# Performance work log

Hardware: AMD Instinct MI355X
Metric: run time of the kernel (lower is better)

Reference implementation:

```python
import jax, jax.numpy as jnp
import numpy as np

N = 1024
DIM = 128
HEADS = 8
DK = DIM // HEADS
EDIM = 16
EPS = 1e-5
NEG = -10000.0


def _lin(k, din, dout):
    return jax.random.normal(k, (din, dout), jnp.float32) * (1.0 / np.sqrt(din))


def setup_inputs() -> dict:
    key = jax.random.key(0)
    ks = jax.random.split(key, 10)
    mask = jax.random.randint(ks[2], (N, N), 0, 2).astype(bool)
    mask = mask | jnp.eye(N, dtype=bool)  # self-loops always valid
    return {
        "x": jax.random.normal(ks[0], (N, DIM), jnp.float32),
        "edge_feat": jax.random.normal(ks[1], (N, N, EDIM), jnp.float32),
        "mask": mask,
        "Wq": _lin(ks[3], DIM, DIM), "bq": jnp.zeros((DIM,), jnp.float32),
        "Wk": _lin(ks[4], DIM, DIM), "bk": jnp.zeros((DIM,), jnp.float32),
        "Wv": _lin(ks[5], DIM, DIM), "bv": jnp.zeros((DIM,), jnp.float32),
        "Wae": _lin(ks[6], EDIM, HEADS), "bae": jnp.zeros((HEADS,), jnp.float32),
        "Wve": _lin(ks[7], EDIM, DIM), "bve": jnp.zeros((DIM,), jnp.float32),
        "Wo": _lin(ks[8], DIM, DIM), "bo": jnp.zeros((DIM,), jnp.float32),
        "gamma": jnp.ones((DIM,), jnp.float32),
        "beta": jnp.zeros((DIM,), jnp.float32),
    }


def reference(x, edge_feat, mask, Wq, bq, Wk, bk, Wv, bv, Wae, bae, Wve, bve, Wo, bo, gamma, beta):
    n, dim = x.shape
    heads = bae.shape[0]
    dk = dim // heads
    # pre-LayerNorm
    mu = jnp.mean(x, axis=-1, keepdims=True)
    var = jnp.mean(jnp.square(x - mu), axis=-1, keepdims=True)
    h = (x - mu) * jax.lax.rsqrt(var + EPS) * gamma + beta
    q = (h @ Wq + bq).reshape(n, heads, dk)
    k = (h @ Wk + bk).reshape(n, heads, dk)
    v = (h @ Wv + bv).reshape(n, heads, dk)
    # attention logits with per-edge additive bias: (n, m, heads)
    att = jnp.einsum('nhd,mhd->nmh', q, k) / np.sqrt(dk).astype(np.float32)
    att = att + edge_feat @ Wae + bae
    att = jnp.where(mask[..., None], att, NEG)
    alpha = jax.nn.softmax(att, axis=1)  # softmax over source nodes m
    # edge-conditioned values: msg_{nm} = v_m + U(e_{nm})
    edge_val = (edge_feat @ Wve + bve).reshape(n, n, heads, dk)
    out = jnp.einsum('nmh,mhd->nhd', alpha, v) + jnp.einsum('nmh,nmhd->nhd', alpha, edge_val)
    out = out.reshape(n, dim) @ Wo + bo
    return x + out
```

## Files before the change

### kernel.cpp

```cpp
#include <hip/hip_runtime.h>
#include <hip/hip_bf16.h>

#define NNODE 1024
#define DIM 128
#define HEADS 8
#define DK 16
#define EDIM 16
#define BN 8
#define MR 32
#define KV_ROW 160
#define H_STRIDE 20
#define EF_ROW 20
#define EF_NSTR 644
#define LOG2E 1.44269504f

__global__ __launch_bounds__(384)
void ln_qkv_kernel(const float* __restrict__ x,
                   const float* __restrict__ Wq, const float* __restrict__ bq,
                   const float* __restrict__ Wk, const float* __restrict__ bk,
                   const float* __restrict__ Wv, const float* __restrict__ bv,
                   const float* __restrict__ gamma, const float* __restrict__ beta,
                   float* __restrict__ qg, float* __restrict__ kg, float* __restrict__ vg) {
    const int n = blockIdx.x;
    const int t = threadIdx.x;
    __shared__ float hrow[DIM];
    __shared__ float part[4];

    float xv = 0.f;
    if (t < 128) {
        xv = x[n * DIM + t];
        float v = xv;
        #pragma unroll
        for (int off = 32; off >= 1; off >>= 1) v += __shfl_xor(v, off);
        if ((t & 63) == 0) part[t >> 6] = v;
    }
    __syncthreads();
    const float mu = (part[0] + part[1]) * (1.0f / DIM);
    const float dx = xv - mu;
    if (t < 128) {
        float v = dx * dx;
        #pragma unroll
        for (int off = 32; off >= 1; off >>= 1) v += __shfl_xor(v, off);
        if ((t & 63) == 0) part[2 + (t >> 6)] = v;
    }
    __syncthreads();
    if (t < 128) {
        const float var = (part[2] + part[3]) * (1.0f / DIM);
        hrow[t] = dx * rsqrtf(var + 1e-5f) * gamma[t] + beta[t];
    }
    __syncthreads();

    const int which = t >> 7;
    const int col = t & 127;
    const float* W = (which == 0) ? Wq : (which == 1) ? Wk : Wv;
    const float* b = (which == 0) ? bq : (which == 1) ? bk : bv;
    float* o       = (which == 0) ? qg : (which == 1) ? kg : vg;
    float acc = b[col];
    #pragma unroll 16
    for (int i = 0; i < DIM; ++i) acc = fmaf(hrow[i], W[i * DIM + col], acc);
    o[n * DIM + col] = acc;
}

__global__ __launch_bounds__(256, 2)
void attn_kernel(const float* __restrict__ qg, const float* __restrict__ kg,
                 const float* __restrict__ vg, const float* __restrict__ ef,
                 const int* __restrict__ mask,
                 const float* __restrict__ Wae, const float* __restrict__ bae,
                 float* __restrict__ acc) {
    const int t = threadIdx.x;
    const int s  = t >> 5;
    const int np = (t >> 3) & 3;
    const int h  = t & 7;
    const int wid = t >> 6, lane = t & 63;
    const int bx = blockIdx.x;
    const int n0 = (bx >> 5) * BN;
    const int mb = (bx & 31) * MR;

    __shared__ float ef_lds[BN * EF_NSTR];
    __shared__ float kv_buf[2 * MR * KV_ROW];
    __shared__ int   mk_lds[BN * 34];

    float* k_lds = kv_buf;
    float* v_lds = kv_buf + MR * KV_ROW;

    #pragma unroll
    for (int r = 0; r < 4; ++r) {
        const int idx = t + 256 * r;
        const int nn = idx >> 7;
        const int mm = (idx >> 2) & 31;
        const int q4 = idx & 3;
        const float4 ev = *(const float4*)(ef + ((size_t)(n0 + nn) * NNODE + mb + mm) * EDIM + q4 * 4);
        *(float4*)&ef_lds[nn * EF_NSTR + mm * EF_ROW + q4 * 4] = ev;
    }
    #pragma unroll
    for (int r = 0; r < 4; ++r) {
        const int idx = t + 256 * r;
        const int mm = idx >> 5, c4 = idx & 31;
        const int hh = c4 >> 2, d4 = c4 & 3;
        const float4 kq = *(const float4*)(kg + (size_t)(mb + mm) * DIM + c4 * 4);
        const float4 vq = *(const float4*)(vg + (size_t)(mb + mm) * DIM + c4 * 4);
        *(float4*)&k_lds[mm * KV_ROW + hh * H_STRIDE + d4 * 4] = kq;
        *(float4*)&v_lds[mm * KV_ROW + hh * H_STRIDE + d4 * 4] = vq;
    }
    {
        const int nn = t >> 5, mm = t & 31;
        mk_lds[nn * 34 + mm] = mask[(size_t)(n0 + nn) * NNODE + (mb + mm)];
    }
    float qreg[2][DK];
    #pragma unroll
    for (int hf = 0; hf < 2; ++hf) {
        const float* qp = qg + (size_t)(n0 + np + 4 * hf) * DIM + h * DK;
        #pragma unroll
        for (int d4 = 0; d4 < 4; ++d4) {
            const float4 qv = *(const float4*)(qp + d4 * 4);
            qreg[hf][d4 * 4 + 0] = qv.x; qreg[hf][d4 * 4 + 1] = qv.y;
            qreg[hf][d4 * 4 + 2] = qv.z; qreg[hf][d4 * 4 + 3] = qv.w;
        }
    }
    float waec[EDIM];
    #pragma unroll
    for (int e = 0; e < EDIM; ++e) waec[e] = Wae[e * HEADS + h] * LOG2E;
    const float baeh = bae[h] * LOG2E;

    float sl[2] = {0.f, 0.f};
    float accv[2][DK], accT[2][EDIM];
    #pragma unroll
    for (int hf = 0; hf < 2; ++hf) {
        #pragma unroll
        for (int d = 0; d < DK; ++d) accv[hf][d] = 0.f;
        #pragma unroll
        for (int e = 0; e < EDIM; ++e) accT[hf][e] = 0.f;
    }

    __syncthreads();

    #pragma unroll
    for (int j = 0; j < 4; ++j) {
        const int m = j * 8 + s;
        float kk[DK], vv[DK];
        const float* kp = &k_lds[m * KV_ROW + h * H_STRIDE];
        const float* vp = &v_lds[m * KV_ROW + h * H_STRIDE];
        #pragma unroll
        for (int d4 = 0; d4 < 4; ++d4) {
            const float4 k4 = *(const float4*)(kp + d4 * 4);
            kk[d4 * 4 + 0] = k4.x; kk[d4 * 4 + 1] = k4.y;
            kk[d4 * 4 + 2] = k4.z; kk[d4 * 4 + 3] = k4.w;
            const float4 v4 = *(const float4*)(vp + d4 * 4);
            vv[d4 * 4 + 0] = v4.x; vv[d4 * 4 + 1] = v4.y;
            vv[d4 * 4 + 2] = v4.z; vv[d4 * 4 + 3] = v4.w;
        }
        #pragma unroll
        for (int hf = 0; hf < 2; ++hf) {
            const int n = np + 4 * hf;
            const float* ep = &ef_lds[n * EF_NSTR + m * EF_ROW];
            float efv[EDIM];
            #pragma unroll
            for (int e4 = 0; e4 < 4; ++e4) {
                const float4 ev = *(const float4*)(ep + e4 * 4);
                efv[e4 * 4 + 0] = ev.x; efv[e4 * 4 + 1] = ev.y;
                efv[e4 * 4 + 2] = ev.z; efv[e4 * 4 + 3] = ev.w;
            }
            float bias = baeh, dot = 0.f;
            #pragma unroll
            for (int e = 0; e < EDIM; ++e) bias = fmaf(efv[e], waec[e], bias);
            #pragma unroll
            for (int d = 0; d < DK; ++d) dot = fmaf(qreg[hf][d], kk[d], dot);
            const float lg = fmaf(dot, 0.25f * LOG2E, bias);
            const float p = mk_lds[n * 34 + m] ? __builtin_amdgcn_exp2f(lg) : 0.f;
            sl[hf] += p;
            #pragma unroll
            for (int d = 0; d < DK; ++d) accv[hf][d] = fmaf(p, vv[d], accv[hf][d]);
            #pragma unroll
            for (int e = 0; e < EDIM; ++e) accT[hf][e] = fmaf(p, efv[e], accT[hf][e]);
        }
    }

    #pragma unroll
    for (int hf = 0; hf < 2; ++hf) {
        sl[hf] += __shfl_xor(sl[hf], 32);
        #pragma unroll
        for (int d = 0; d < DK; ++d) accv[hf][d] += __shfl_xor(accv[hf][d], 32);
        #pragma unroll
        for (int e = 0; e < EDIM; ++e) accT[hf][e] += __shfl_xor(accT[hf][e], 32);
    }
    __syncthreads();
    float* red = kv_buf;
    if (lane < 32) {
        float* rp = &red[((wid * 4 + np) * 8 + h) * 66];
        #pragma unroll
        for (int hf = 0; hf < 2; ++hf) {
            rp[hf * 33 + 0] = sl[hf];
            #pragma unroll
            for (int d = 0; d < DK; ++d) rp[hf * 33 + 1 + d] = accv[hf][d];
            #pragma unroll
            for (int e = 0; e < EDIM; ++e) rp[hf * 33 + 17 + e] = accT[hf][e];
        }
    }
    __syncthreads();
    for (int v = t; v < BN * HEADS * 33; v += 256) {
        const int n = v / 264;
        const int rem = v - n * 264;
        const int hh = rem / 33;
        const int idx = rem - hh * 33;
        const int nnp = n & 3, hf = n >> 2;
        float sum = 0.f;
        #pragma unroll
        for (int w = 0; w < 4; ++w)
            sum += red[((w * 4 + nnp) * 8 + hh) * 66 + hf * 33 + idx];
        atomicAdd(&acc[((size_t)(n0 + n) * HEADS + hh) * 33 + idx], sum);
    }
}

__global__ __launch_bounds__(128)
void final_kernel(const float* __restrict__ acc,
                  const float* __restrict__ Wve, const float* __restrict__ bve,
                  const float* __restrict__ x,
                  const float* __restrict__ Wo, const float* __restrict__ bo,
                  float* __restrict__ out) {
    const int n = blockIdx.x, t = threadIdx.x;
    __shared__ float ab[HEADS * 33];
    __shared__ float orow[DIM];
    for (int u = t; u < HEADS * 33; u += 128) ab[u] = acc[(size_t)n * HEADS * 33 + u];
    __syncthreads();
    const int col = t, hh = col >> 4, dd = col & 15;
    const float slv = ab[hh * 33];
    float acc2 = 0.f;
    #pragma unroll
    for (int e = 0; e < EDIM; ++e) acc2 = fmaf(ab[hh * 33 + 17 + e], Wve[e * DIM + col], acc2);
    orow[col] = (ab[hh * 33 + 1 + dd] + acc2) / slv + bve[col];
    __syncthreads();
    float o = bo[col] + x[(size_t)n * DIM + col];
    #pragma unroll 16
    for (int i = 0; i < DIM; ++i) o = fmaf(orow[i], Wo[i * DIM + col], o);
    out[(size_t)n * DIM + col] = o;
}

extern "C" void kernel_launch(void* const* d_in, const int* in_sizes, int n_in,
                              void* d_out, int out_size, void* d_ws, size_t ws_size,
                              hipStream_t stream) {
    const float* x     = (const float*)d_in[0];
    const float* ef    = (const float*)d_in[1];
    const int*   mask  = (const int*)d_in[2];
    const float* Wq    = (const float*)d_in[3];
    const float* bq    = (const float*)d_in[4];
    const float* Wk    = (const float*)d_in[5];
    const float* bk    = (const float*)d_in[6];
    const float* Wv    = (const float*)d_in[7];
    const float* bv    = (const float*)d_in[8];
    const float* Wae   = (const float*)d_in[9];
    const float* bae   = (const float*)d_in[10];
    const float* Wve   = (const float*)d_in[11];
    const float* bve   = (const float*)d_in[12];
    const float* Wo    = (const float*)d_in[13];
    const float* bo    = (const float*)d_in[14];
    const float* gamma = (const float*)d_in[15];
    const float* beta  = (const float*)d_in[16];

    float* ws = (float*)d_ws;
    float* accb = ws;
    float* qg   = ws + 270336;
    float* kg   = qg + (size_t)NNODE * DIM;
    float* vg   = kg + (size_t)NNODE * DIM;

    hipMemsetAsync(accb, 0, (size_t)NNODE * HEADS * 33 * sizeof(float), stream);
    ln_qkv_kernel<<<NNODE, 384, 0, stream>>>(x, Wq, bq, Wk, bk, Wv, bv, gamma, beta, qg, kg, vg);
    attn_kernel<<<(NNODE / BN) * 32, 256, 0, stream>>>(qg, kg, vg, ef, mask, Wae, bae, accb);
    final_kernel<<<NNODE, 128, 0, stream>>>(accb, Wve, bve, x, Wo, bo, (float*)d_out);
}
```

Baseline: 184.8 us.

## Loop attention blocks over 8 source chunks with smaller LDS tiles and higher occupancy

Each attention block now walks 8 chunks of 16 source nodes instead of handling one 32-node tile. The grid drops from 4096 to 1024 blocks, so fewer partial results get atomically accumulated. LDS per block shrinks and launch bounds ask for 4 blocks per CU to raise occupancy, at the cost of a sync per chunk and no overlap between loads and compute. The projection GEMV loops also split their FMA chains into two accumulators to add ILP.

```diff
diff --git a/kernel.cpp b/kernel.cpp
--- a/kernel.cpp
+++ b/kernel.cpp
@@ -7,12 +7,18 @@
 #define DK 16
 #define EDIM 16
 #define BN 8
-#define MR 32
+#define MR 16
+#define NCH 8
 #define KV_ROW 160
 #define H_STRIDE 20
 #define EF_ROW 20
-#define EF_NSTR 644
+#define EF_NSTR 324
+#define MK_STR 17
 #define LOG2E 1.44269504f
+
+#define SMEM_F 8448
+#define KV_OFF 2592
+#define MK_OFF 7712
 
 __global__ __launch_bounds__(384)
 void ln_qkv_kernel(const float* __restrict__ x,
@@ -55,13 +61,16 @@
     const float* W = (which == 0) ? Wq : (which == 1) ? Wk : Wv;
     const float* b = (which == 0) ? bq : (which == 1) ? bk : bv;
     float* o       = (which == 0) ? qg : (which == 1) ? kg : vg;
-    float acc = b[col];
-    #pragma unroll 16
-    for (int i = 0; i < DIM; ++i) acc = fmaf(hrow[i], W[i * DIM + col], acc);
-    o[n * DIM + col] = acc;
-}
-
-__global__ __launch_bounds__(256, 2)
+    float a0 = b[col], a1 = 0.f;
+    #pragma unroll 8
+    for (int i = 0; i < DIM; i += 2) {
+        a0 = fmaf(hrow[i],     W[i * DIM + col],       a0);
+        a1 = fmaf(hrow[i + 1], W[(i + 1) * DIM + col], a1);
+    }
+    o[n * DIM + col] = a0 + a1;
+}
+
+__global__ __launch_bounds__(256, 4)
 void attn_kernel(const float* __restrict__ qg, const float* __restrict__ kg,
                  const float* __restrict__ vg, const float* __restrict__ ef,
                  const int* __restrict__ mask,
@@ -73,39 +82,15 @@
     const int h  = t & 7;
     const int wid = t >> 6, lane = t & 63;
     const int bx = blockIdx.x;
-    const int n0 = (bx >> 5) * BN;
-    const int mb = (bx & 31) * MR;
-
-    __shared__ float ef_lds[BN * EF_NSTR];
-    __shared__ float kv_buf[2 * MR * KV_ROW];
-    __shared__ int   mk_lds[BN * 34];
-
-    float* k_lds = kv_buf;
-    float* v_lds = kv_buf + MR * KV_ROW;
-
-    #pragma unroll
-    for (int r = 0; r < 4; ++r) {
-        const int idx = t + 256 * r;
-        const int nn = idx >> 7;
-        const int mm = (idx >> 2) & 31;
-        const int q4 = idx & 3;
-        const float4 ev = *(const float4*)(ef + ((size_t)(n0 + nn) * NNODE + mb + mm) * EDIM + q4 * 4);
-        *(float4*)&ef_lds[nn * EF_NSTR + mm * EF_ROW + q4 * 4] = ev;
-    }
-    #pragma unroll
-    for (int r = 0; r < 4; ++r) {
-        const int idx = t + 256 * r;
-        const int mm = idx >> 5, c4 = idx & 31;
-        const int hh = c4 >> 2, d4 = c4 & 3;
-        const float4 kq = *(const float4*)(kg + (size_t)(mb + mm) * DIM + c4 * 4);
-        const float4 vq = *(const float4*)(vg + (size_t)(mb + mm) * DIM + c4 * 4);
-        *(float4*)&k_lds[mm * KV_ROW + hh * H_STRIDE + d4 * 4] = kq;
-        *(float4*)&v_lds[mm * KV_ROW + hh * H_STRIDE + d4 * 4] = vq;
-    }
-    {
-        const int nn = t >> 5, mm = t & 31;
-        mk_lds[nn * 34 + mm] = mask[(size_t)(n0 + nn) * NNODE + (mb + mm)];
-    }
+    const int n0  = (bx >> 3) * BN;
+    const int mb0 = (bx & 7) * (MR * NCH);
+
+    __shared__ float smem[SMEM_F];
+    float* ef_lds = smem;
+    float* k_lds  = smem + KV_OFF;
+    float* v_lds  = smem + KV_OFF + MR * KV_ROW;
+    int*   mk_lds = (int*)(smem + MK_OFF);
+
     float qreg[2][DK];
     #pragma unroll
     for (int hf = 0; hf < 2; ++hf) {
@@ -132,46 +117,75 @@
         for (int e = 0; e < EDIM; ++e) accT[hf][e] = 0.f;
     }
 
-    __syncthreads();
-
-    #pragma unroll
-    for (int j = 0; j < 4; ++j) {
-        const int m = j * 8 + s;
-        float kk[DK], vv[DK];
-        const float* kp = &k_lds[m * KV_ROW + h * H_STRIDE];
-        const float* vp = &v_lds[m * KV_ROW + h * H_STRIDE];
-        #pragma unroll
-        for (int d4 = 0; d4 < 4; ++d4) {
-            const float4 k4 = *(const float4*)(kp + d4 * 4);
-            kk[d4 * 4 + 0] = k4.x; kk[d4 * 4 + 1] = k4.y;
-            kk[d4 * 4 + 2] = k4.z; kk[d4 * 4 + 3] = k4.w;
-            const float4 v4 = *(const float4*)(vp + d4 * 4);
-            vv[d4 * 4 + 0] = v4.x; vv[d4 * 4 + 1] = v4.y;
-            vv[d4 * 4 + 2] = v4.z; vv[d4 * 4 + 3] = v4.w;
-        }
-        #pragma unroll
-        for (int hf = 0; hf < 2; ++hf) {
-            const int n = np + 4 * hf;
-            const float* ep = &ef_lds[n * EF_NSTR + m * EF_ROW];
-            float efv[EDIM];
-            #pragma unroll
-            for (int e4 = 0; e4 < 4; ++e4) {
-                const float4 ev = *(const float4*)(ep + e4 * 4);
-                efv[e4 * 4 + 0] = ev.x; efv[e4 * 4 + 1] = ev.y;
-                efv[e4 * 4 + 2] = ev.z; efv[e4 * 4 + 3] = ev.w;
+    #pragma unroll 1
+    for (int c = 0; c < NCH; ++c) {
+        const int mb = mb0 + c * MR;
+        if (c) __syncthreads();
+
+        #pragma unroll
+        for (int r = 0; r < 2; ++r) {
+            const int idx = t + 256 * r;
+            const int nn = idx >> 6;
+            const int mm = (idx >> 2) & 15;
+            const int q4 = idx & 3;
+            const float4 ev = *(const float4*)(ef + ((size_t)(n0 + nn) * NNODE + mb + mm) * EDIM + q4 * 4);
+            *(float4*)&ef_lds[nn * EF_NSTR + mm * EF_ROW + q4 * 4] = ev;
+        }
+        #pragma unroll
+        for (int r = 0; r < 2; ++r) {
+            const int idx = t + 256 * r;
+            const int mm = idx >> 5, c4 = idx & 31;
+            const int hh = c4 >> 2, d4 = c4 & 3;
+            const float4 kq = *(const float4*)(kg + (size_t)(mb + mm) * DIM + c4 * 4);
+            const float4 vq = *(const float4*)(vg + (size_t)(mb + mm) * DIM + c4 * 4);
+            *(float4*)&k_lds[mm * KV_ROW + hh * H_STRIDE + d4 * 4] = kq;
+            *(float4*)&v_lds[mm * KV_ROW + hh * H_STRIDE + d4 * 4] = vq;
+        }
+        if (t < BN * MR) {
+            const int nn = t >> 4, mm = t & 15;
+            mk_lds[nn * MK_STR + mm] = mask[(size_t)(n0 + nn) * NNODE + (mb + mm)];
+        }
+        __syncthreads();
+
+        #pragma unroll
+        for (int j = 0; j < 2; ++j) {
+            const int m = j * 8 + s;
+            float kk[DK], vv[DK];
+            const float* kp = &k_lds[m * KV_ROW + h * H_STRIDE];
+            const float* vp = &v_lds[m * KV_ROW + h * H_STRIDE];
+            #pragma unroll
+            for (int d4 = 0; d4 < 4; ++d4) {
+                const float4 k4 = *(const float4*)(kp + d4 * 4);
+                kk[d4 * 4 + 0] = k4.x; kk[d4 * 4 + 1] = k4.y;
+                kk[d4 * 4 + 2] = k4.z; kk[d4 * 4 + 3] = k4.w;
+                const float4 v4 = *(const float4*)(vp + d4 * 4);
+                vv[d4 * 4 + 0] = v4.x; vv[d4 * 4 + 1] = v4.y;
+                vv[d4 * 4 + 2] = v4.z; vv[d4 * 4 + 3] = v4.w;
             }
-            float bias = baeh, dot = 0.f;
-            #pragma unroll
-            for (int e = 0; e < EDIM; ++e) bias = fmaf(efv[e], waec[e], bias);
-            #pragma unroll
-            for (int d = 0; d < DK; ++d) dot = fmaf(qreg[hf][d], kk[d], dot);
-            const float lg = fmaf(dot, 0.25f * LOG2E, bias);
-            const float p = mk_lds[n * 34 + m] ? __builtin_amdgcn_exp2f(lg) : 0.f;
-            sl[hf] += p;
-            #pragma unroll
-            for (int d = 0; d < DK; ++d) accv[hf][d] = fmaf(p, vv[d], accv[hf][d]);
-            #pragma unroll
-            for (int e = 0; e < EDIM; ++e) accT[hf][e] = fmaf(p, efv[e], accT[hf][e]);
+            #pragma unroll
+            for (int hf = 0; hf < 2; ++hf) {
+                const int n = np + 4 * hf;
+                const float* ep = &ef_lds[n * EF_NSTR + m * EF_ROW];
+                float efv[EDIM];
+                #pragma unroll
+                for (int e4 = 0; e4 < 4; ++e4) {
+                    const float4 ev = *(const float4*)(ep + e4 * 4);
+                    efv[e4 * 4 + 0] = ev.x; efv[e4 * 4 + 1] = ev.y;
+                    efv[e4 * 4 + 2] = ev.z; efv[e4 * 4 + 3] = ev.w;
+                }
+                float bias = baeh, dot = 0.f;
+                #pragma unroll
+                for (int e = 0; e < EDIM; ++e) bias = fmaf(efv[e], waec[e], bias);
+                #pragma unroll
+                for (int d = 0; d < DK; ++d) dot = fmaf(qreg[hf][d], kk[d], dot);
+                const float lg = fmaf(dot, 0.25f * LOG2E, bias);
+                const float p = mk_lds[n * MK_STR + m] ? __builtin_amdgcn_exp2f(lg) : 0.f;
+                sl[hf] += p;
+                #pragma unroll
+                for (int d = 0; d < DK; ++d) accv[hf][d] = fmaf(p, vv[d], accv[hf][d]);
+                #pragma unroll
+                for (int e = 0; e < EDIM; ++e) accT[hf][e] = fmaf(p, efv[e], accT[hf][e]);
+            }
         }
     }
 
@@ -184,7 +198,7 @@
         for (int e = 0; e < EDIM; ++e) accT[hf][e] += __shfl_xor(accT[hf][e], 32);
     }
     __syncthreads();
-    float* red = kv_buf;
+    float* red = smem;
     if (lane < 32) {
         float* rp = &red[((wid * 4 + np) * 8 + h) * 66];
         #pragma unroll
@@ -229,10 +243,13 @@
     for (int e = 0; e < EDIM; ++e) acc2 = fmaf(ab[hh * 33 + 17 + e], Wve[e * DIM + col], acc2);
     orow[col] = (ab[hh * 33 + 1 + dd] + acc2) / slv + bve[col];
     __syncthreads();
-    float o = bo[col] + x[(size_t)n * DIM + col];
-    #pragma unroll 16
-    for (int i = 0; i < DIM; ++i) o = fmaf(orow[i], Wo[i * DIM + col], o);
-    out[(size_t)n * DIM + col] = o;
+    float o0 = bo[col] + x[(size_t)n * DIM + col], o1 = 0.f;
+    #pragma unroll 8
+    for (int i = 0; i < DIM; i += 2) {
+        o0 = fmaf(orow[i],     Wo[i * DIM + col],       o0);
+        o1 = fmaf(orow[i + 1], Wo[(i + 1) * DIM + col], o1);
+    }
+    out[(size_t)n * DIM + col] = o0 + o1;
 }
 
 extern "C" void kernel_launch(void* const* d_in, const int* in_sizes, int n_in,
@@ -264,6 +281,6 @@
 
     hipMemsetAsync(accb, 0, (size_t)NNODE * HEADS * 33 * sizeof(float), stream);
     ln_qkv_kernel<<<NNODE, 384, 0, stream>>>(x, Wq, bq, Wk, bk, Wv, bv, gamma, beta, qg, kg, vg);
-    attn_kernel<<<(NNODE / BN) * 32, 256, 0, stream>>>(qg, kg, vg, ef, mask, Wae, bae, accb);
+    attn_kernel<<<(NNODE / BN) * (NNODE / (MR * NCH)), 256, 0, stream>>>(qg, kg, vg, ef, mask, Wae, bae, accb);
     final_kernel<<<NNODE, 128, 0, stream>>>(accb, Wve, bve, x, Wo, bo, (float*)d_out);
 }
```

New measurement: 391.6 us. 2.12x slower.
